# Kernel tuning notes

Measured on AMD Instinct MI355X. Metric: run time of the kernel, lower is better.

The kernel has to match this reference:

```python
import jax, jax.numpy as jnp
import numpy as np

N_NODES = 100000
N_EDGES = 3200000
IN_DIM = 11
HID = 32


def setup_inputs() -> dict:
    key = jax.random.key(0)
    ks = jax.random.split(key, 12)
    inp = {
        "x": jax.random.normal(ks[0], (N_NODES, IN_DIM), dtype=jnp.float32),
        "edge_index": jax.random.randint(ks[1], (2, N_EDGES), 0, N_NODES, dtype=jnp.int32),
        "batch": jnp.zeros((N_NODES,), dtype=jnp.int32),
        # GCNConv layer 1 (11 -> 32)
        "W1": jax.random.normal(ks[2], (IN_DIM, HID), dtype=jnp.float32) / np.sqrt(IN_DIM),
        "b1": jnp.zeros((HID,), dtype=jnp.float32),
        # GCNConv layer 2 (32 -> 32)
        "W2": jax.random.normal(ks[3], (HID, HID), dtype=jnp.float32) / np.sqrt(HID),
        "b2": jnp.zeros((HID,), dtype=jnp.float32),
        # output MLP: 32 -> 16 -> 1
        "Wo1": jax.random.normal(ks[4], (HID, HID // 2), dtype=jnp.float32) / np.sqrt(HID),
        "bo1": jnp.zeros((HID // 2,), dtype=jnp.float32),
        "Wo2": jax.random.normal(ks[5], (HID // 2, 1), dtype=jnp.float32) / np.sqrt(HID // 2),
        "bo2": jnp.zeros((1,), dtype=jnp.float32),
    }
    return inp


def _gcn_norm(edge_index, n_nodes):
    # Add self-loops and compute symmetric normalization (PyG GCNConv default).
    loops = jnp.arange(n_nodes, dtype=edge_index.dtype)
    src = jnp.concatenate([edge_index[0], loops])
    dst = jnp.concatenate([edge_index[1], loops])
    ones = jnp.ones_like(dst, dtype=jnp.float32)
    deg = jax.ops.segment_sum(ones, dst, num_segments=n_nodes)  # degree of A+I on target side
    dinv = jax.lax.rsqrt(deg)  # deg >= 1 thanks to self-loops
    norm = dinv[src] * dinv[dst]  # [E+N]
    return src, dst, norm


def _gcn_conv(x, W, b, src, dst, norm, n_nodes):
    xw = x @ W                                   # transform first (small dim)
    msg = norm[:, None] * xw[src]                # gather + scale  [E+N, H]
    agg = jax.ops.segment_sum(msg, dst, num_segments=n_nodes)  # scatter-add
    return agg + b


def reference(x, edge_index, batch, W1, b1, W2, b2, Wo1, bo1, Wo2, bo2):
    n = x.shape[0]
    src, dst, norm = _gcn_norm(edge_index, n)
    h = jax.nn.relu(_gcn_conv(x, W1, b1, src, dst, norm, n))
    # F.dropout(training=self.training) is identity in eval mode
    h = jax.nn.relu(_gcn_conv(h, W2, b2, src, dst, norm, n))
    h = jax.nn.elu(h @ Wo1 + bo1)
    out = h @ Wo2 + bo2
    return out.squeeze(-1)  # [N]
```

## Files before the change

### kernel.cpp

```cpp
#include <hip/hip_runtime.h>
#include <hip/hip_fp16.h>
#include <math.h>

#define N_NODES 100000
#define N_EDGES 3200000
#define IN_DIM 11
#define HID 32
#define HID2 16
#define SCHUNK 100352
#define BINSHIFT 8
#define BINSZ 256
#define NB 391
#define CHUNK 4096
#define NBC 782

__global__ __launch_bounds__(256) void k_hist(const int* __restrict__ ei,
                                              int* __restrict__ cnthist) {
    __shared__ int h[NB];
    int t = threadIdx.x;
    for (int i = t; i < NB; i += 256) h[i] = 0;
    __syncthreads();
    int b0 = blockIdx.x * CHUNK;
    int e1 = b0 + CHUNK; if (e1 > N_EDGES) e1 = N_EDGES;
    for (int e = b0 + t; e < e1; e += 256)
        atomicAdd(&h[ei[N_EDGES + e] >> BINSHIFT], 1);
    __syncthreads();
    for (int i = t; i < NB; i += 256)
        cnthist[i * NBC + blockIdx.x] = h[i];
}

__global__ __launch_bounds__(256) void k_colscan(int* __restrict__ cnthist,
                                                 int* __restrict__ colsum) {
    __shared__ int tmp[256];
    int i = blockIdx.x;
    int t = threadIdx.x;
    int v[4];
    int s4 = 0;
#pragma unroll
    for (int u = 0; u < 4; ++u) {
        int idx = t * 4 + u;
        v[u] = (idx < NBC) ? cnthist[i * NBC + idx] : 0;
        s4 += v[u];
    }
    tmp[t] = s4;
    __syncthreads();
    for (int off = 1; off < 256; off <<= 1) {
        int u = (t >= off) ? tmp[t - off] : 0;
        __syncthreads();
        tmp[t] += u;
        __syncthreads();
    }
    int base = tmp[t] - s4;
#pragma unroll
    for (int u = 0; u < 4; ++u) {
        int idx = t * 4 + u;
        if (idx < NBC) cnthist[i * NBC + idx] = base;
        base += v[u];
    }
    if (t == 255) colsum[i] = tmp[255];
}

__global__ __launch_bounds__(512) void k_scanbins(const int* __restrict__ colsum,
                                                  int* __restrict__ binbase) {
    __shared__ int tmp[512];
    int t = threadIdx.x;
    int v = (t < NB) ? colsum[t] : 0;
    tmp[t] = v;
    __syncthreads();
    for (int off = 1; off < 512; off <<= 1) {
        int u = (t >= off) ? tmp[t - off] : 0;
        __syncthreads();
        tmp[t] += u;
        __syncthreads();
    }
    if (t < NB) binbase[t] = tmp[t] - v;
    if (t == 0) binbase[NB] = N_EDGES;
}

__global__ __launch_bounds__(256) void k_binscatter(const int* __restrict__ ei,
                                                    const int* __restrict__ binbase,
                                                    const int* __restrict__ cnthist,
                                                    unsigned* __restrict__ binbuf) {
    __shared__ int h[NB];
    __shared__ int base[NB];
    int t = threadIdx.x;
    for (int i = t; i < NB; i += 256) {
        base[i] = binbase[i] + cnthist[i * NBC + blockIdx.x];
        h[i] = 0;
    }
    __syncthreads();
    int b0 = blockIdx.x * CHUNK;
    int e1 = b0 + CHUNK; if (e1 > N_EDGES) e1 = N_EDGES;
    for (int e = b0 + t; e < e1; e += 256) {
        int d = ei[N_EDGES + e];
        int s = ei[e];
        int b = d >> BINSHIFT;
        int p = base[b] + atomicAdd(&h[b], 1);
        binbuf[p] = (unsigned)s | ((unsigned)(d & (BINSZ - 1)) << 17);
    }
}

__global__ __launch_bounds__(512) void k_binfill(const unsigned* __restrict__ binbuf,
                                                 const int* __restrict__ binbase,
                                                 int* __restrict__ rowstart,
                                                 float* __restrict__ dinv,
                                                 int* __restrict__ csr_src) {
    int b = blockIdx.x, t = threadIdx.x;
    __shared__ int cnt[BINSZ], rloc[BINSZ], cur[BINSZ], tmp[BINSZ];
    int ebeg = binbase[b], eend = binbase[b + 1];
    if (t < BINSZ) cnt[t] = 0;
    __syncthreads();
    for (int e = ebeg + t; e < eend; e += 512)
        atomicAdd(&cnt[binbuf[e] >> 17], 1);
    __syncthreads();
    int c = 0;
    if (t < BINSZ) { c = cnt[t]; tmp[t] = c; }
    __syncthreads();
    for (int off = 1; off < BINSZ; off <<= 1) {
        int u = (t < BINSZ && t >= off) ? tmp[t - off] : 0;
        __syncthreads();
        if (t < BINSZ) tmp[t] += u;
        __syncthreads();
    }
    if (t < BINSZ) {
        rloc[t] = tmp[t] - c;
        cur[t] = 0;
        int node = b * BINSZ + t;
        if (node < N_NODES) {
            rowstart[node] = ebeg + rloc[t];
            dinv[node] = rsqrtf((float)c + 1.0f);
        }
    }
    if (b == 0 && t == 0) rowstart[N_NODES] = N_EDGES;
    __syncthreads();
    for (int e = ebeg + t; e < eend; e += 512) {
        unsigned vv = binbuf[e];
        int dl = vv >> 17;
        int s = (int)(vv & 0x1FFFFu);
        int p = ebeg + rloc[dl] + atomicAdd(&cur[dl], 1);
        csr_src[p] = s;
    }
}

__global__ void k_xw1(const float* __restrict__ x, const float* __restrict__ W1,
                      const float* __restrict__ dinv, __half* __restrict__ xwh) {
    int t = blockIdx.x * blockDim.x + threadIdx.x;
    int node = t >> 5;
    int j = t & 31;
    __shared__ float sW[IN_DIM * HID];
    __shared__ float sx[8 * IN_DIM];
    for (int i = threadIdx.x; i < IN_DIM * HID; i += 256) sW[i] = W1[i];
    int base = blockIdx.x * 8;
    if (threadIdx.x < 8 * IN_DIM) sx[threadIdx.x] = x[base * IN_DIM + threadIdx.x];
    __syncthreads();
    int ln = node - base;
    float acc = 0.0f;
#pragma unroll
    for (int k = 0; k < IN_DIM; ++k)
        acc += sx[ln * IN_DIM + k] * sW[k * HID + j];
    xwh[t] = __float2half(dinv[node] * acc);
}

__device__ __forceinline__ void accum8(float* __restrict__ acc, const uint4 v) {
    float2 f0 = __half22float2(*(const __half2*)&v.x);
    float2 f1 = __half22float2(*(const __half2*)&v.y);
    float2 f2 = __half22float2(*(const __half2*)&v.z);
    float2 f3 = __half22float2(*(const __half2*)&v.w);
    acc[0] += f0.x; acc[1] += f0.y;
    acc[2] += f1.x; acc[3] += f1.y;
    acc[4] += f2.x; acc[5] += f2.y;
    acc[6] += f3.x; acc[7] += f3.y;
}

__device__ __forceinline__ void edge_accum8(int beg, int end, int q, int oj,
                                            const int* __restrict__ csr_src,
                                            const __half* __restrict__ xwh,
                                            float* __restrict__ acc) {
#pragma unroll
    for (int k = 0; k < 8; ++k) acc[k] = 0.0f;
    int e = beg;
    for (; e + 32 <= end; e += 32) {
        int s0 = csr_src[e + q];
        int s1 = csr_src[e + 8 + q];
        int s2 = csr_src[e + 16 + q];
        int s3 = csr_src[e + 24 + q];
        uint4 v0 = *(const uint4*)(xwh + ((s0 << 5) | oj));
        uint4 v1 = *(const uint4*)(xwh + ((s1 << 5) | oj));
        uint4 v2 = *(const uint4*)(xwh + ((s2 << 5) | oj));
        uint4 v3 = *(const uint4*)(xwh + ((s3 << 5) | oj));
        accum8(acc, v0); accum8(acc, v1); accum8(acc, v2); accum8(acc, v3);
    }
    if (e + 16 <= end) {
        int s0 = csr_src[e + q];
        int s1 = csr_src[e + 8 + q];
        uint4 v0 = *(const uint4*)(xwh + ((s0 << 5) | oj));
        uint4 v1 = *(const uint4*)(xwh + ((s1 << 5) | oj));
        accum8(acc, v0); accum8(acc, v1);
        e += 16;
    }
    if (e + 8 <= end) {
        int s0 = csr_src[e + q];
        uint4 v0 = *(const uint4*)(xwh + ((s0 << 5) | oj));
        accum8(acc, v0);
        e += 8;
    }
    if (e + q < end) {
        int s0 = csr_src[e + q];
        uint4 v0 = *(const uint4*)(xwh + ((s0 << 5) | oj));
        accum8(acc, v0);
    }
#pragma unroll
    for (int m = 4; m <= 16; m <<= 1) {
#pragma unroll
        for (int k = 0; k < 8; ++k) acc[k] += __shfl_xor(acc[k], m);
    }
}

__global__ __launch_bounds__(256) void k_gather_xw2(const int* __restrict__ rowstart,
                                                    const float* __restrict__ dinv,
                                                    const int* __restrict__ csr_src,
                                                    const __half* __restrict__ xwh1,
                                                    const float* __restrict__ b1,
                                                    const float* __restrict__ W2,
                                                    __half* __restrict__ xwh2) {
    __shared__ float sW2[HID * HID];
    __shared__ float sA[8][33];
    __shared__ float sH[8][33];
    for (int i = threadIdx.x; i < HID * HID; i += 256) sW2[i] = W2[i];

    int ln = threadIdx.x >> 5;
    int node = blockIdx.x * 8 + ln;
    int l = threadIdx.x & 31;
    int q = l >> 2;
    int oj = (l & 3) << 3;

    float acc[8];
    edge_accum8(rowstart[node], rowstart[node + 1], q, oj, csr_src, xwh1, acc);
    if (q == 0) {
#pragma unroll
        for (int k = 0; k < 8; ++k) sA[ln][oj + k] = acc[k];
    }
    __syncthreads();

    int j = l;
    float dd = dinv[node];
    float hv = dd * (sA[ln][j] + __half2float(xwh1[node * HID + j])) + b1[j];
    sH[ln][j] = hv > 0.0f ? hv : 0.0f;
    __syncthreads();

    float a2 = 0.0f;
#pragma unroll
    for (int k = 0; k < HID; ++k) a2 += sH[ln][k] * sW2[k * HID + j];
    xwh2[node * HID + j] = __float2half(dd * a2);
}

__global__ __launch_bounds__(256) void k_gather_mlp(const int* __restrict__ rowstart,
                                                    const float* __restrict__ dinv,
                                                    const int* __restrict__ csr_src,
                                                    const __half* __restrict__ xwh,
                                                    const float* __restrict__ b2,
                                                    const float* __restrict__ Wo1,
                                                    const float* __restrict__ bo1,
                                                    const float* __restrict__ Wo2,
                                                    const float* __restrict__ bo2,
                                                    float* __restrict__ out) {
    __shared__ float sW1[HID * HID2];
    __shared__ float sb1[HID2];
    __shared__ float sW2v[HID2];
    __shared__ float sb2[HID];
    __shared__ float sA[8][33];
    __shared__ float sH[8][33];
    for (int i = threadIdx.x; i < HID * HID2; i += 256) sW1[i] = Wo1[i];
    if (threadIdx.x < HID2) {
        sb1[threadIdx.x] = bo1[threadIdx.x];
        sW2v[threadIdx.x] = Wo2[threadIdx.x];
    }
    if (threadIdx.x < HID) sb2[threadIdx.x] = b2[threadIdx.x];

    int ln = threadIdx.x >> 5;
    int node = blockIdx.x * 8 + ln;
    int l = threadIdx.x & 31;
    int q = l >> 2;
    int oj = (l & 3) << 3;

    float acc[8];
    edge_accum8(rowstart[node], rowstart[node + 1], q, oj, csr_src, xwh, acc);
    if (q == 0) {
#pragma unroll
        for (int k = 0; k < 8; ++k) sA[ln][oj + k] = acc[k];
    }
    __syncthreads();

    int j = l;
    float dd = dinv[node];
    float hv = dd * (sA[ln][j] + __half2float(xwh[node * HID + j])) + sb2[j];
    sH[ln][j] = hv > 0.0f ? hv : 0.0f;
    __syncthreads();

    float val = 0.0f;
    if (j < HID2) {
        float a = sb1[j];
#pragma unroll
        for (int k = 0; k < HID; ++k) a += sH[ln][k] * sW1[k * HID2 + j];
        a = a > 0.0f ? a : (expf(a) - 1.0f);
        val = a * sW2v[j];
    }
#pragma unroll
    for (int d = 16; d >= 1; d >>= 1) val += __shfl_down(val, d, 32);
    if (j == 0) out[node] = val + bo2[0];
}

extern "C" void kernel_launch(void* const* d_in, const int* in_sizes, int n_in,
                              void* d_out, int out_size, void* d_ws, size_t ws_size,
                              hipStream_t stream) {
    const float* x   = (const float*)d_in[0];
    const int*   ei  = (const int*)d_in[1];
    const float* W1  = (const float*)d_in[3];
    const float* b1  = (const float*)d_in[4];
    const float* W2  = (const float*)d_in[5];
    const float* b2  = (const float*)d_in[6];
    const float* Wo1 = (const float*)d_in[7];
    const float* bo1 = (const float*)d_in[8];
    const float* Wo2 = (const float*)d_in[9];
    const float* bo2 = (const float*)d_in[10];
    float* out = (float*)d_out;

    int*      colsum   = (int*)d_ws;
    int*      binbase  = colsum + 512;
    int*      rowstart = binbase + 512;
    float*    dinv     = (float*)(rowstart + SCHUNK);
    int*      csr_src  = (int*)(dinv + SCHUNK);
    unsigned* binbuf   = (unsigned*)(csr_src + N_EDGES);
    __half*   XWH1     = (__half*)(binbuf + N_EDGES);
    __half*   XWH2     = XWH1 + (size_t)N_NODES * HID;
    int*      cnthist  = csr_src;

    const int BT = 256;
    int gNH  = (N_NODES * HID + BT - 1) / BT;
    int gG   = N_NODES / 8;

    k_hist      <<<NBC, BT, 0, stream>>>(ei, cnthist);
    k_colscan   <<<NB, BT, 0, stream>>>(cnthist, colsum);
    k_scanbins  <<<1, 512, 0, stream>>>(colsum, binbase);
    k_binscatter<<<NBC, BT, 0, stream>>>(ei, binbase, cnthist, binbuf);
    k_binfill   <<<NB, 512, 0, stream>>>(binbuf, binbase, rowstart, dinv, csr_src);

    k_xw1<<<gNH, BT, 0, stream>>>(x, W1, dinv, XWH1);
    k_gather_xw2<<<gG, BT, 0, stream>>>(rowstart, dinv, csr_src, XWH1, b1, W2, XWH2);

    k_gather_mlp<<<gG, BT, 0, stream>>>(rowstart, dinv, csr_src, XWH2,
                                        b2, Wo1, bo1, Wo2, bo2, out);
}
```

Measured before the change: 267.0 us.

## Locally sort edges per chunk before bin scatter and split binfill across two blocks

The bin-scatter kernel now counting-sorts each chunk's edges by bin in shared memory and then writes them out contiguously, so global writes to the bin buffer are coalesced instead of scattered. The histogram kernel reads destination indices as int4 vectors. The bin-fill kernel is split into two blocks per bin, each handling half the destination rows, to double parallelism. In exchange, binscatter uses much more shared memory (lower occupancy), and each binfill half re-reads the whole bin.

```diff
diff --git a/kernel.cpp b/kernel.cpp
--- a/kernel.cpp
+++ b/kernel.cpp
@@ -12,7 +12,7 @@
 #define BINSZ 256
 #define NB 391
 #define CHUNK 4096
-#define NBC 782
+#define NCH 782
 
 __global__ __launch_bounds__(256) void k_hist(const int* __restrict__ ei,
                                               int* __restrict__ cnthist) {
@@ -21,12 +21,17 @@
     for (int i = t; i < NB; i += 256) h[i] = 0;
     __syncthreads();
     int b0 = blockIdx.x * CHUNK;
-    int e1 = b0 + CHUNK; if (e1 > N_EDGES) e1 = N_EDGES;
-    for (int e = b0 + t; e < e1; e += 256)
-        atomicAdd(&h[ei[N_EDGES + e] >> BINSHIFT], 1);
+    int n = N_EDGES - b0; if (n > CHUNK) n = CHUNK;
+    for (int e = t * 4; e < n; e += 1024) {
+        int4 d4 = *(const int4*)(ei + N_EDGES + b0 + e);
+        atomicAdd(&h[d4.x >> BINSHIFT], 1);
+        atomicAdd(&h[d4.y >> BINSHIFT], 1);
+        atomicAdd(&h[d4.z >> BINSHIFT], 1);
+        atomicAdd(&h[d4.w >> BINSHIFT], 1);
+    }
     __syncthreads();
     for (int i = t; i < NB; i += 256)
-        cnthist[i * NBC + blockIdx.x] = h[i];
+        cnthist[i * NCH + blockIdx.x] = h[i];
 }
 
 __global__ __launch_bounds__(256) void k_colscan(int* __restrict__ cnthist,
@@ -39,7 +44,7 @@
 #pragma unroll
     for (int u = 0; u < 4; ++u) {
         int idx = t * 4 + u;
-        v[u] = (idx < NBC) ? cnthist[i * NBC + idx] : 0;
+        v[u] = (idx < NCH) ? cnthist[i * NCH + idx] : 0;
         s4 += v[u];
     }
     tmp[t] = s4;
@@ -54,7 +59,7 @@
 #pragma unroll
     for (int u = 0; u < 4; ++u) {
         int idx = t * 4 + u;
-        if (idx < NBC) cnthist[i * NBC + idx] = base;
+        if (idx < NCH) cnthist[i * NCH + idx] = base;
         base += v[u];
     }
     if (t == 255) colsum[i] = tmp[255];
@@ -77,68 +82,99 @@
     if (t == 0) binbase[NB] = N_EDGES;
 }
 
-__global__ __launch_bounds__(256) void k_binscatter(const int* __restrict__ ei,
+__global__ __launch_bounds__(512) void k_binscatter(const int* __restrict__ ei,
                                                     const int* __restrict__ binbase,
                                                     const int* __restrict__ cnthist,
                                                     unsigned* __restrict__ binbuf) {
-    __shared__ int h[NB];
-    __shared__ int base[NB];
-    int t = threadIdx.x;
-    for (int i = t; i < NB; i += 256) {
-        base[i] = binbase[i] + cnthist[i * NBC + blockIdx.x];
-        h[i] = 0;
-    }
-    __syncthreads();
+    __shared__ unsigned short sbin[CHUNK];
+    __shared__ unsigned char  sdl[CHUNK];
+    __shared__ unsigned       srecS[CHUNK];
+    __shared__ unsigned short sbinS[CHUNK];
+    __shared__ int h[NB], rl[NB], gb[NB];
+    __shared__ int tmp[512];
+    int t = threadIdx.x;
     int b0 = blockIdx.x * CHUNK;
-    int e1 = b0 + CHUNK; if (e1 > N_EDGES) e1 = N_EDGES;
-    for (int e = b0 + t; e < e1; e += 256) {
-        int d = ei[N_EDGES + e];
-        int s = ei[e];
+    int n = N_EDGES - b0; if (n > CHUNK) n = CHUNK;
+    for (int i = t; i < NB; i += 512) h[i] = 0;
+    __syncthreads();
+    for (int e = t; e < n; e += 512) {
+        int d = ei[N_EDGES + b0 + e];
         int b = d >> BINSHIFT;
-        int p = base[b] + atomicAdd(&h[b], 1);
-        binbuf[p] = (unsigned)s | ((unsigned)(d & (BINSZ - 1)) << 17);
-    }
-}
-
-__global__ __launch_bounds__(512) void k_binfill(const unsigned* __restrict__ binbuf,
+        sbin[e] = (unsigned short)b;
+        sdl[e]  = (unsigned char)(d & (BINSZ - 1));
+        atomicAdd(&h[b], 1);
+    }
+    __syncthreads();
+    int c = (t < NB) ? h[t] : 0;
+    tmp[t] = c;
+    __syncthreads();
+    for (int off = 1; off < 512; off <<= 1) {
+        int u = (t >= off) ? tmp[t - off] : 0;
+        __syncthreads();
+        tmp[t] += u;
+        __syncthreads();
+    }
+    if (t < NB) {
+        rl[t] = tmp[t] - c;
+        gb[t] = binbase[t] + cnthist[t * NCH + blockIdx.x];
+        h[t] = 0;
+    }
+    __syncthreads();
+    for (int e = t; e < n; e += 512) {
+        int s = ei[b0 + e];
+        int b = sbin[e];
+        int p = rl[b] + atomicAdd(&h[b], 1);
+        srecS[p] = (unsigned)s | ((unsigned)sdl[e] << 17);
+        sbinS[p] = (unsigned short)b;
+    }
+    __syncthreads();
+    for (int p = t; p < n; p += 512) {
+        int b = sbinS[p];
+        binbuf[gb[b] + (p - rl[b])] = srecS[p];
+    }
+}
+
+__global__ __launch_bounds__(256) void k_binfill(const unsigned* __restrict__ binbuf,
                                                  const int* __restrict__ binbase,
                                                  int* __restrict__ rowstart,
                                                  float* __restrict__ dinv,
                                                  int* __restrict__ csr_src) {
-    int b = blockIdx.x, t = threadIdx.x;
+    int bb = blockIdx.x;
+    int b = bb >> 1;
+    int half = bb & 1;
+    int t = threadIdx.x;
     __shared__ int cnt[BINSZ], rloc[BINSZ], cur[BINSZ], tmp[BINSZ];
     int ebeg = binbase[b], eend = binbase[b + 1];
-    if (t < BINSZ) cnt[t] = 0;
-    __syncthreads();
-    for (int e = ebeg + t; e < eend; e += 512)
+    cnt[t] = 0;
+    __syncthreads();
+    for (int e = ebeg + t; e < eend; e += 256)
         atomicAdd(&cnt[binbuf[e] >> 17], 1);
     __syncthreads();
-    int c = 0;
-    if (t < BINSZ) { c = cnt[t]; tmp[t] = c; }
-    __syncthreads();
-    for (int off = 1; off < BINSZ; off <<= 1) {
-        int u = (t < BINSZ && t >= off) ? tmp[t - off] : 0;
-        __syncthreads();
-        if (t < BINSZ) tmp[t] += u;
-        __syncthreads();
-    }
-    if (t < BINSZ) {
-        rloc[t] = tmp[t] - c;
-        cur[t] = 0;
-        int node = b * BINSZ + t;
-        if (node < N_NODES) {
-            rowstart[node] = ebeg + rloc[t];
-            dinv[node] = rsqrtf((float)c + 1.0f);
-        }
-    }
-    if (b == 0 && t == 0) rowstart[N_NODES] = N_EDGES;
-    __syncthreads();
-    for (int e = ebeg + t; e < eend; e += 512) {
+    int c = cnt[t];
+    tmp[t] = c;
+    __syncthreads();
+    for (int off = 1; off < 256; off <<= 1) {
+        int u = (t >= off) ? tmp[t - off] : 0;
+        __syncthreads();
+        tmp[t] += u;
+        __syncthreads();
+    }
+    rloc[t] = tmp[t] - c;
+    cur[t] = 0;
+    int node = b * BINSZ + t;
+    if ((t >> 7) == half && node < N_NODES) {
+        rowstart[node] = ebeg + rloc[t];
+        dinv[node] = rsqrtf((float)c + 1.0f);
+    }
+    if (bb == 0 && t == 0) rowstart[N_NODES] = N_EDGES;
+    __syncthreads();
+    for (int e = ebeg + t; e < eend; e += 256) {
         unsigned vv = binbuf[e];
         int dl = vv >> 17;
-        int s = (int)(vv & 0x1FFFFu);
-        int p = ebeg + rloc[dl] + atomicAdd(&cur[dl], 1);
-        csr_src[p] = s;
+        if ((dl >> 7) == half) {
+            int p = ebeg + rloc[dl] + atomicAdd(&cur[dl], 1);
+            csr_src[p] = (int)(vv & 0x1FFFFu);
+        }
     }
 }
 
@@ -339,11 +375,11 @@
     int gNH  = (N_NODES * HID + BT - 1) / BT;
     int gG   = N_NODES / 8;
 
-    k_hist      <<<NBC, BT, 0, stream>>>(ei, cnthist);
+    k_hist      <<<NCH, BT, 0, stream>>>(ei, cnthist);
     k_colscan   <<<NB, BT, 0, stream>>>(cnthist, colsum);
     k_scanbins  <<<1, 512, 0, stream>>>(colsum, binbase);
-    k_binscatter<<<NBC, BT, 0, stream>>>(ei, binbase, cnthist, binbuf);
-    k_binfill   <<<NB, 512, 0, stream>>>(binbuf, binbase, rowstart, dinv, csr_src);
+    k_binscatter<<<NCH, 512, 0, stream>>>(ei, binbase, cnthist, binbuf);
+    k_binfill   <<<2 * NB, BT, 0, stream>>>(binbuf, binbase, rowstart, dinv, csr_src);
 
     k_xw1<<<gNH, BT, 0, stream>>>(x, W1, dinv, XWH1);
     k_gather_xw2<<<gG, BT, 0, stream>>>(rowstart, dinv, csr_src, XWH1, b1, W2, XWH2);
```

Measured after the change: 252.6 us. 1.06x faster.
